# Kernel tuning notes

Measured on AMD Instinct MI355X. Metric: run time of the kernel, lower is better.

The kernel has to match this reference:

```python
import jax, jax.numpy as jnp
import numpy as np

N_AGENTS = 64
_adj = np.ones((N_AGENTS, N_AGENTS)) - np.eye(N_AGENTS)
SEND_NP, RECV_NP = np.where(_adj)  # 4032 directed edges, no self-loops
N_EDGES = SEND_NP.shape[0]

D_NODE = 16
H = 64
D_OUT = 16
N_TYPES = 2
BATCH = 128


def _glorot(key, shape):
    fan_in, fan_out = shape[0], shape[1]
    lim = np.sqrt(6.0 / (fan_in + fan_out)).astype(np.float32)
    return jax.random.uniform(key, shape, jnp.float32, -lim, lim)


def setup_inputs() -> dict:
    key = jax.random.key(0)
    ks = jax.random.split(key, 16)
    inp = {
        "node_states": jax.random.normal(ks[0], (BATCH, N_AGENTS, 1, D_NODE), jnp.float32),
        "edge_types": jax.random.uniform(ks[1], (BATCH, N_EDGES, N_TYPES + 1, 1), jnp.float32),
        # edge encoder 0: MLP(32 -> 64 -> 64)
        "e0_w1": _glorot(ks[2], (2 * D_NODE, H)), "e0_b1": jnp.zeros((H,), jnp.float32),
        "e0_w2": _glorot(ks[3], (H, H)), "e0_b2": jnp.zeros((H,), jnp.float32),
        # edge encoder 1
        "e1_w1": _glorot(ks[4], (2 * D_NODE, H)), "e1_b1": jnp.zeros((H,), jnp.float32),
        "e1_w2": _glorot(ks[5], (H, H)), "e1_b2": jnp.zeros((H,), jnp.float32),
        # node decoder: MLP(16+64 -> 64 -> 16)
        "nd_w1": _glorot(ks[6], (D_NODE + H, H)), "nd_b1": jnp.zeros((H,), jnp.float32),
        "nd_w2": _glorot(ks[7], (H, D_OUT)), "nd_b2": jnp.zeros((D_OUT,), jnp.float32),
    }
    return inp


def _mlp2(x, w1, b1, w2, b2):
    h = jax.nn.relu(x @ w1 + b1)
    return jax.nn.relu(h @ w2 + b2)


def reference(node_states, edge_types,
              e0_w1, e0_b1, e0_w2, e0_b2,
              e1_w1, e1_b1, e1_w2, e1_b2,
              nd_w1, nd_b1, nd_w2, nd_b2):
    send = jnp.asarray(SEND_NP)
    recv = jnp.asarray(RECV_NP)
    # NodeAggregator: gather sender/receiver states to edges -> [B, E, 1, 2D]
    edge_msg = jnp.concatenate([node_states[:, send], node_states[:, recv]], axis=-1)
    # per-edge-type MLP encode, concat along axis 2 -> [B, E, T, H]
    enc0 = _mlp2(edge_msg, e0_w1, e0_b1, e0_w2, e0_b2)
    enc1 = _mlp2(edge_msg, e1_w1, e1_b1, e1_w2, e1_b2)
    encoded = jnp.concatenate([enc0, enc1], axis=2)
    # masked sum over edge types (skip type-0 'no edge') -> [B, E, 1, H]
    edge_msg_sum = jnp.sum(encoded * edge_types[:, :, 1:, :], axis=2, keepdims=True)
    # EdgeAggregator: scatter-sum edge messages to receiver nodes -> [B, N, 1, H]
    node_msg = jax.ops.segment_sum(
        edge_msg_sum.swapaxes(0, 1), recv, num_segments=N_AGENTS).swapaxes(0, 1)
    # decode
    node_state = jnp.concatenate([node_states, node_msg], axis=-1)  # [B, N, 1, D+H]
    return _mlp2(node_state, nd_w1, nd_b1, nd_w2, nd_b2)
```

## Files before the change

### kernel.cpp

```cpp
#include <hip/hip_runtime.h>
#include <hip/hip_fp16.h>


typedef _Float16 hf;
typedef __attribute__((ext_vector_type(8))) _Float16 v8hf;
typedef __attribute__((ext_vector_type(4))) float fv4;

union ABh { v8hf v; __half2 h[4]; };

__global__ __launch_bounds__(256, 4) void fused_kernel(
    const float* __restrict__ ns, const float* __restrict__ et,
    const float* __restrict__ e0w1, const float* __restrict__ e0b1,
    const float* __restrict__ e0w2, const float* __restrict__ e0b2,
    const float* __restrict__ e1w1, const float* __restrict__ e1b1,
    const float* __restrict__ e1w2, const float* __restrict__ e1b2,
    const float* __restrict__ ndw1, const float* __restrict__ ndb1,
    const float* __restrict__ ndw2, const float* __restrict__ ndb2,
    float* __restrict__ out)
{
  __shared__ __align__(16) _Float16 PlH[2*64*72];
  __shared__ __align__(16) _Float16 QbH[2*8*64];
  __shared__ float ETl[2*8*64];
  __shared__ __align__(16) _Float16 XDH[24*104];
  _Float16* XD  = XDH;
  _Float16* HD2 = XDH + 8*104;

  int t = threadIdx.x;
  int b = blockIdx.x >> 3, rg = blockIdx.x & 7, r0 = rg*8;
  int w = t >> 6, lane = t & 63, quad = lane >> 4, col = lane & 15;

  const __half2 z2 = __float22half2_rn(make_float2(0.f, 0.f));
  const v8hf zero8 = {};

  float xnv = 0.f;
  if (t < 128) xnv = ns[(b*64 + r0 + (t >> 4))*16 + (t & 15)];
  float ev0[2], ev1[2];
  int es[2], erl[2];
#pragma unroll
  for (int i = 0; i < 2; ++i) {
    int idx = i*256 + t;
    int s = idx >> 3, rl = idx & 7;
    es[i] = s; erl[i] = rl;
    int r = r0 + rl;
    float v0 = 0.f, v1 = 0.f;
    if (s != r) {
      int pos = r - (r > s ? 1 : 0);
      const float* base = et + (b*4032 + s*63 + pos)*3;
      v0 = base[1]; v1 = base[2];
    }
    ev0[i] = v0; ev1[i] = v1;
  }

  {
    ABh a;
    if (quad < 2) {
      const float* xr = ns + (b*64 + w*16 + col)*16 + quad*8;
      float4 x0 = *(const float4*)xr;
      float4 x1 = *(const float4*)(xr + 4);
      a.h[0] = __float22half2_rn(make_float2(x0.x, x0.y));
      a.h[1] = __float22half2_rn(make_float2(x0.z, x0.w));
      a.h[2] = __float22half2_rn(make_float2(x1.x, x1.y));
      a.h[3] = __float22half2_rn(make_float2(x1.z, x1.w));
    } else {
      a.h[0] = a.h[1] = a.h[2] = a.h[3] = z2;
    }
    bool qwave = (w == (rg >> 1));
#pragma unroll 1
    for (int enc = 0; enc < 2; ++enc) {
      const float* w1 = enc ? e1w1 : e0w1;
      const float* b1 = enc ? e1b1 : e0b1;
#pragma unroll
      for (int ht = 0; ht < 4; ++ht) {
        int cc = ht*16 + col;
        ABh bb;
        if (quad < 2) {
#pragma unroll
          for (int j = 0; j < 4; ++j) {
            float f0 = w1[(quad*8 + 2*j    )*64 + cc];
            float f1 = w1[(quad*8 + 2*j + 1)*64 + cc];
            bb.h[j] = __float22half2_rn(make_float2(f0, f1));
          }
        } else {
          bb.h[0] = bb.h[1] = bb.h[2] = bb.h[3] = z2;
        }
        fv4 acc = {0.f, 0.f, 0.f, 0.f};
        acc = __builtin_amdgcn_mfma_f32_16x16x32_f16(a.v, bb.v, acc, 0, 0, 0);
        hf* pd = PlH + enc*4608 + (w*16 + quad*4)*72 + cc;
        pd[0*72] = (hf)acc[0];
        pd[1*72] = (hf)acc[1];
        pd[2*72] = (hf)acc[2];
        pd[3*72] = (hf)acc[3];
      }
      if (qwave) {
#pragma unroll
        for (int ht = 0; ht < 4; ++ht) {
          int cc = ht*16 + col;
          ABh bb;
          if (quad < 2) {
#pragma unroll
            for (int j = 0; j < 4; ++j) {
              float f0 = w1[(16 + quad*8 + 2*j    )*64 + cc];
              float f1 = w1[(16 + quad*8 + 2*j + 1)*64 + cc];
              bb.h[j] = __float22half2_rn(make_float2(f0, f1));
            }
          } else {
            bb.h[0] = bb.h[1] = bb.h[2] = bb.h[3] = z2;
          }
          fv4 acc = {0.f, 0.f, 0.f, 0.f};
          acc = __builtin_amdgcn_mfma_f32_16x16x32_f16(a.v, bb.v, acc, 0, 0, 0);
          float b1v = b1[cc];
#pragma unroll
          for (int rr = 0; rr < 4; ++rr) {
            int local = quad*4 + rr;
            if ((local >> 3) == (rg & 1))
              QbH[enc*512 + (local & 7)*64 + cc] = (hf)(acc[rr] + b1v);
          }
        }
      }
    }
  }
  if (t < 128) {
    int rl = t >> 4, k = t & 15;
    XD[rl*104 + k] = (hf)xnv;
    XD[rl*104 + 80 + k] = (hf)0.f;
  }
#pragma unroll
  for (int i = 0; i < 2; ++i) {
    ETl[erl[i]*64 + es[i]] = ev0[i];
    ETl[512 + erl[i]*64 + es[i]] = ev1[i];
  }
  __syncthreads();

  float msgacc[2][4] = {{0.f,0.f,0.f,0.f},{0.f,0.f,0.f,0.f}};

#pragma unroll 1
  for (int enc = 0; enc < 2; ++enc) {
    const float* w2 = enc ? e1w2 : e0w2;
    const float* b2 = enc ? e1b2 : e0b2;
    v8hf bfr[4][2];
    float b2v[4];
#pragma unroll
    for (int nt = 0; nt < 4; ++nt) {
#pragma unroll
      for (int kk = 0; kk < 2; ++kk) {
        const float* base = w2 + (kk*32 + quad*8)*64 + nt*16 + col;
        ABh bb;
        bb.h[0] = __float22half2_rn(make_float2(base[0*64], base[1*64]));
        bb.h[1] = __float22half2_rn(make_float2(base[2*64], base[3*64]));
        bb.h[2] = __float22half2_rn(make_float2(base[4*64], base[5*64]));
        bb.h[3] = __float22half2_rn(make_float2(base[6*64], base[7*64]));
        bfr[nt][kk] = bb.v;
      }
      b2v[nt] = b2[nt*16 + col];
    }
#pragma unroll 1
    for (int rli = 0; rli < 2; ++rli) {
      int rl = w*2 + rli;
      const hf* qrow = QbH + (enc*8 + rl)*64;
      v8hf q0 = *(const v8hf*)(qrow + quad*8);
      v8hf q1 = *(const v8hf*)(qrow + 32 + quad*8);
      const float* etrow = ETl + (enc*8 + rl)*64;
#pragma unroll 2
      for (int st = 0; st < 4; ++st) {
        const hf* prow = PlH + enc*4608 + (st*16 + col)*72 + quad*8;
        v8hf p0 = *(const v8hf*)prow;
        v8hf p1 = *(const v8hf*)(prow + 32);
        v8hf s0 = __builtin_elementwise_max(p0 + q0, zero8);
        v8hf s1 = __builtin_elementwise_max(p1 + q1, zero8);
        float4 etv = *(const float4*)(etrow + st*16 + quad*4);
#pragma unroll
        for (int nt = 0; nt < 4; ++nt) {
          fv4 acc = {b2v[nt], b2v[nt], b2v[nt], b2v[nt]};
          acc = __builtin_amdgcn_mfma_f32_16x16x32_f16(s0, bfr[nt][0], acc, 0, 0, 0);
          acc = __builtin_amdgcn_mfma_f32_16x16x32_f16(s1, bfr[nt][1], acc, 0, 0, 0);
          float m = msgacc[rli][nt];
          m += etv.x * fmaxf(acc[0], 0.f);
          m += etv.y * fmaxf(acc[1], 0.f);
          m += etv.z * fmaxf(acc[2], 0.f);
          m += etv.w * fmaxf(acc[3], 0.f);
          msgacc[rli][nt] = m;
        }
      }
    }
  }
#pragma unroll
  for (int rli = 0; rli < 2; ++rli) {
#pragma unroll
    for (int nt = 0; nt < 4; ++nt) {
      float v = msgacc[rli][nt];
      v += __shfl_xor(v, 16);
      v += __shfl_xor(v, 32);
      if (lane < 16) XD[(w*2 + rli)*104 + 16 + nt*16 + lane] = (hf)v;
    }
  }
  __syncthreads();

  if (w == 0) {
    ABh xa[3];
    const hf* xrow = XD + col*104;
#pragma unroll
    for (int kk = 0; kk < 3; ++kk) xa[kk].v = *(const v8hf*)(xrow + kk*32 + quad*8);
#pragma unroll
    for (int ht = 0; ht < 4; ++ht) {
      int cc = ht*16 + col;
      float bias = ndb1[cc];
      fv4 acc = {bias, bias, bias, bias};
#pragma unroll
      for (int kk = 0; kk < 3; ++kk) {
        ABh bb;
#pragma unroll
        for (int j = 0; j < 4; ++j) {
          int rA = kk*32 + quad*8 + 2*j;
          int rB = rA + 1;
          float f0 = ndw1[(rA < 80 ? rA : 79)*64 + cc] * (rA < 80 ? 1.f : 0.f);
          float f1 = ndw1[(rB < 80 ? rB : 79)*64 + cc] * (rB < 80 ? 1.f : 0.f);
          bb.h[j] = __float22half2_rn(make_float2(f0, f1));
        }
        acc = __builtin_amdgcn_mfma_f32_16x16x32_f16(xa[kk].v, bb.v, acc, 0, 0, 0);
      }
      if (quad < 2) {
#pragma unroll
        for (int rr = 0; rr < 4; ++rr)
          HD2[(quad*4 + rr)*104 + cc] = (hf)fmaxf(acc[rr], 0.f);
      }
    }
    const hf* hrow = HD2 + col*104;
    v8hf ha0 = *(const v8hf*)(hrow + quad*8);
    v8hf ha1 = *(const v8hf*)(hrow + 32 + quad*8);
    ABh b20, b21;
#pragma unroll
    for (int j = 0; j < 4; ++j) {
      float f0 = ndw2[(quad*8 + 2*j    )*16 + col];
      float f1 = ndw2[(quad*8 + 2*j + 1)*16 + col];
      b20.h[j] = __float22half2_rn(make_float2(f0, f1));
      float g0 = ndw2[(32 + quad*8 + 2*j    )*16 + col];
      float g1 = ndw2[(32 + quad*8 + 2*j + 1)*16 + col];
      b21.h[j] = __float22half2_rn(make_float2(g0, g1));
    }
    float bias2 = ndb2[col];
    fv4 acc2 = {bias2, bias2, bias2, bias2};
    acc2 = __builtin_amdgcn_mfma_f32_16x16x32_f16(ha0, b20.v, acc2, 0, 0, 0);
    acc2 = __builtin_amdgcn_mfma_f32_16x16x32_f16(ha1, b21.v, acc2, 0, 0, 0);
    if (quad < 2) {
#pragma unroll
      for (int rr = 0; rr < 4; ++rr) {
        int rl = quad*4 + rr;
        out[(b*64 + r0 + rl)*16 + col] = fmaxf(acc2[rr], 0.f);
      }
    }
  }
}

extern "C" void kernel_launch(void* const* d_in, const int* in_sizes, int n_in,
                              void* d_out, int out_size, void* d_ws, size_t ws_size,
                              hipStream_t stream) {
  const float* ns   = (const float*)d_in[0];
  const float* et   = (const float*)d_in[1];
  const float* e0w1 = (const float*)d_in[2];
  const float* e0b1 = (const float*)d_in[3];
  const float* e0w2 = (const float*)d_in[4];
  const float* e0b2 = (const float*)d_in[5];
  const float* e1w1 = (const float*)d_in[6];
  const float* e1b1 = (const float*)d_in[7];
  const float* e1w2 = (const float*)d_in[8];
  const float* e1b2 = (const float*)d_in[9];
  const float* ndw1 = (const float*)d_in[10];
  const float* ndb1 = (const float*)d_in[11];
  const float* ndw2 = (const float*)d_in[12];
  const float* ndb2 = (const float*)d_in[13];

  fused_kernel<<<1024, 256, 0, stream>>>(ns, et,
                                         e0w1, e0b1, e0w2, e0b2,
                                         e1w1, e1b1, e1w2, e1b2,
                                         ndw1, ndb1, ndw2, ndb2,
                                         (float*)d_out);
}
```

Baseline: 109.1 us.

## Stage weight matrices into LDS as transposed fp16 via coalesced float4 loads

Replaces the per-lane strided scalar global loads and fp16 conversions of all MLP weight matrices with a cooperative staging step. The block loads each matrix with coalesced float4 reads, converts it once to fp16 in a transposed, padded LDS layout, and the MFMA B operands are then read as single 16-byte LDS vectors. This targets uncoalesced global traffic and redundant conversions in every wave. In exchange it adds extra LDS (a new WB buffer), reuses PlH for the decoder weights, and inserts several more __syncthreads barriers, which may lower occupancy.

```diff
diff --git a/kernel.cpp b/kernel.cpp
--- a/kernel.cpp
+++ b/kernel.cpp
@@ -22,6 +22,7 @@
   __shared__ __align__(16) _Float16 QbH[2*8*64];
   __shared__ float ETl[2*8*64];
   __shared__ __align__(16) _Float16 XDH[24*104];
+  __shared__ __align__(16) _Float16 WB[2*64*40 + 16];
   _Float16* XD  = XDH;
   _Float16* HD2 = XDH + 8*104;
 
@@ -35,12 +36,10 @@
   float xnv = 0.f;
   if (t < 128) xnv = ns[(b*64 + r0 + (t >> 4))*16 + (t & 15)];
   float ev0[2], ev1[2];
-  int es[2], erl[2];
 #pragma unroll
   for (int i = 0; i < 2; ++i) {
     int idx = i*256 + t;
     int s = idx >> 3, rl = idx & 7;
-    es[i] = s; erl[i] = rl;
     int r = r0 + rl;
     float v0 = 0.f, v1 = 0.f;
     if (s != r) {
@@ -50,6 +49,24 @@
     }
     ev0[i] = v0; ev1[i] = v1;
   }
+
+#pragma unroll
+  for (int it = 0; it < 4; ++it) {
+    int idx = it*256 + t;
+    int enc = idx >> 9, rem = idx & 511;
+    int k = rem >> 4, h0 = (rem & 15)*4;
+    const float* w1 = enc ? e1w1 : e0w1;
+    float4 v = *(const float4*)(w1 + k*64 + h0);
+    hf* dst = WB + enc*2560 + h0*40 + k;
+    dst[0*40] = (hf)v.x; dst[1*40] = (hf)v.y; dst[2*40] = (hf)v.z; dst[3*40] = (hf)v.w;
+  }
+#pragma unroll
+  for (int d = 0; d < 4; ++d) {
+    int z = t*4 + d;
+    WB[(z >> 3)*40 + 32 + (z & 7)] = (hf)0.f;
+  }
+  if (t < 16) WB[5120 + t] = (hf)0.f;
+  __syncthreads();
 
   {
     ABh a;
@@ -67,24 +84,13 @@
     bool qwave = (w == (rg >> 1));
 #pragma unroll 1
     for (int enc = 0; enc < 2; ++enc) {
-      const float* w1 = enc ? e1w1 : e0w1;
       const float* b1 = enc ? e1b1 : e0b1;
 #pragma unroll
       for (int ht = 0; ht < 4; ++ht) {
         int cc = ht*16 + col;
-        ABh bb;
-        if (quad < 2) {
-#pragma unroll
-          for (int j = 0; j < 4; ++j) {
-            float f0 = w1[(quad*8 + 2*j    )*64 + cc];
-            float f1 = w1[(quad*8 + 2*j + 1)*64 + cc];
-            bb.h[j] = __float22half2_rn(make_float2(f0, f1));
-          }
-        } else {
-          bb.h[0] = bb.h[1] = bb.h[2] = bb.h[3] = z2;
-        }
+        v8hf bb = *(const v8hf*)(WB + enc*2560 + cc*40 + quad*8);
         fv4 acc = {0.f, 0.f, 0.f, 0.f};
-        acc = __builtin_amdgcn_mfma_f32_16x16x32_f16(a.v, bb.v, acc, 0, 0, 0);
+        acc = __builtin_amdgcn_mfma_f32_16x16x32_f16(a.v, bb, acc, 0, 0, 0);
         hf* pd = PlH + enc*4608 + (w*16 + quad*4)*72 + cc;
         pd[0*72] = (hf)acc[0];
         pd[1*72] = (hf)acc[1];
@@ -95,19 +101,9 @@
 #pragma unroll
         for (int ht = 0; ht < 4; ++ht) {
           int cc = ht*16 + col;
-          ABh bb;
-          if (quad < 2) {
-#pragma unroll
-            for (int j = 0; j < 4; ++j) {
-              float f0 = w1[(16 + quad*8 + 2*j    )*64 + cc];
-              float f1 = w1[(16 + quad*8 + 2*j + 1)*64 + cc];
-              bb.h[j] = __float22half2_rn(make_float2(f0, f1));
-            }
-          } else {
-            bb.h[0] = bb.h[1] = bb.h[2] = bb.h[3] = z2;
-          }
+          v8hf bb = *(const v8hf*)(WB + enc*2560 + cc*40 + 16 + quad*8);
           fv4 acc = {0.f, 0.f, 0.f, 0.f};
-          acc = __builtin_amdgcn_mfma_f32_16x16x32_f16(a.v, bb.v, acc, 0, 0, 0);
+          acc = __builtin_amdgcn_mfma_f32_16x16x32_f16(a.v, bb, acc, 0, 0, 0);
           float b1v = b1[cc];
 #pragma unroll
           for (int rr = 0; rr < 4; ++rr) {
@@ -119,6 +115,16 @@
       }
     }
   }
+  __syncthreads();
+
+#pragma unroll
+  for (int it = 0; it < 4; ++it) {
+    int idx = it*256 + t;
+    int k = idx >> 4, n0 = (idx & 15)*4;
+    float4 v = *(const float4*)(e0w2 + k*64 + n0);
+    hf* dst = WB + n0*72 + k;
+    dst[0*72] = (hf)v.x; dst[1*72] = (hf)v.y; dst[2*72] = (hf)v.z; dst[3*72] = (hf)v.w;
+  }
   if (t < 128) {
     int rl = t >> 4, k = t & 15;
     XD[rl*104 + k] = (hf)xnv;
@@ -126,8 +132,10 @@
   }
 #pragma unroll
   for (int i = 0; i < 2; ++i) {
-    ETl[erl[i]*64 + es[i]] = ev0[i];
-    ETl[512 + erl[i]*64 + es[i]] = ev1[i];
+    int idx = i*256 + t;
+    int s = idx >> 3, rl = idx & 7;
+    ETl[rl*64 + s] = ev0[i];
+    ETl[512 + rl*64 + s] = ev1[i];
   }
   __syncthreads();
 
@@ -135,22 +143,26 @@
 
 #pragma unroll 1
   for (int enc = 0; enc < 2; ++enc) {
-    const float* w2 = enc ? e1w2 : e0w2;
+    if (enc == 1) {
+      __syncthreads();
+#pragma unroll
+      for (int it = 0; it < 4; ++it) {
+        int idx = it*256 + t;
+        int k = idx >> 4, n0 = (idx & 15)*4;
+        float4 v = *(const float4*)(e1w2 + k*64 + n0);
+        hf* dst = WB + n0*72 + k;
+        dst[0*72] = (hf)v.x; dst[1*72] = (hf)v.y; dst[2*72] = (hf)v.z; dst[3*72] = (hf)v.w;
+      }
+      __syncthreads();
+    }
     const float* b2 = enc ? e1b2 : e0b2;
     v8hf bfr[4][2];
     float b2v[4];
 #pragma unroll
     for (int nt = 0; nt < 4; ++nt) {
 #pragma unroll
-      for (int kk = 0; kk < 2; ++kk) {
-        const float* base = w2 + (kk*32 + quad*8)*64 + nt*16 + col;
-        ABh bb;
-        bb.h[0] = __float22half2_rn(make_float2(base[0*64], base[1*64]));
-        bb.h[1] = __float22half2_rn(make_float2(base[2*64], base[3*64]));
-        bb.h[2] = __float22half2_rn(make_float2(base[4*64], base[5*64]));
-        bb.h[3] = __float22half2_rn(make_float2(base[6*64], base[7*64]));
-        bfr[nt][kk] = bb.v;
-      }
+      for (int kk = 0; kk < 2; ++kk)
+        bfr[nt][kk] = *(const v8hf*)(WB + (nt*16 + col)*72 + kk*32 + quad*8);
       b2v[nt] = b2[nt*16 + col];
     }
 #pragma unroll 1
@@ -195,6 +207,28 @@
   }
   __syncthreads();
 
+#pragma unroll
+  for (int it = 0; it < 5; ++it) {
+    int idx = it*256 + t;
+    int k = idx >> 4, n0 = (idx & 15)*4;
+    float4 v = *(const float4*)(ndw1 + k*64 + n0);
+    hf* dst = PlH + n0*104 + k;
+    dst[0*104] = (hf)v.x; dst[1*104] = (hf)v.y; dst[2*104] = (hf)v.z; dst[3*104] = (hf)v.w;
+  }
+#pragma unroll
+  for (int d = 0; d < 4; ++d) {
+    int z = t*4 + d;
+    PlH[(z >> 4)*104 + 80 + (z & 15)] = (hf)0.f;
+  }
+  {
+    int k = t >> 2, o0 = (t & 3)*4;
+    float4 v = *(const float4*)(ndw2 + k*16 + o0);
+    hf* nd2 = PlH + 6656;
+    nd2[(o0+0)*72 + k] = (hf)v.x; nd2[(o0+1)*72 + k] = (hf)v.y;
+    nd2[(o0+2)*72 + k] = (hf)v.z; nd2[(o0+3)*72 + k] = (hf)v.w;
+  }
+  __syncthreads();
+
   if (w == 0) {
     ABh xa[3];
     const hf* xrow = XD + col*104;
@@ -207,16 +241,8 @@
       fv4 acc = {bias, bias, bias, bias};
 #pragma unroll
       for (int kk = 0; kk < 3; ++kk) {
-        ABh bb;
-#pragma unroll
-        for (int j = 0; j < 4; ++j) {
-          int rA = kk*32 + quad*8 + 2*j;
-          int rB = rA + 1;
-          float f0 = ndw1[(rA < 80 ? rA : 79)*64 + cc] * (rA < 80 ? 1.f : 0.f);
-          float f1 = ndw1[(rB < 80 ? rB : 79)*64 + cc] * (rB < 80 ? 1.f : 0.f);
-          bb.h[j] = __float22half2_rn(make_float2(f0, f1));
-        }
-        acc = __builtin_amdgcn_mfma_f32_16x16x32_f16(xa[kk].v, bb.v, acc, 0, 0, 0);
+        v8hf bb = *(const v8hf*)(PlH + cc*104 + kk*32 + quad*8);
+        acc = __builtin_amdgcn_mfma_f32_16x16x32_f16(xa[kk].v, bb, acc, 0, 0, 0);
       }
       if (quad < 2) {
 #pragma unroll
@@ -227,20 +253,13 @@
     const hf* hrow = HD2 + col*104;
     v8hf ha0 = *(const v8hf*)(hrow + quad*8);
     v8hf ha1 = *(const v8hf*)(hrow + 32 + quad*8);
-    ABh b20, b21;
-#pragma unroll
-    for (int j = 0; j < 4; ++j) {
-      float f0 = ndw2[(quad*8 + 2*j    )*16 + col];
-      float f1 = ndw2[(quad*8 + 2*j + 1)*16 + col];
-      b20.h[j] = __float22half2_rn(make_float2(f0, f1));
-      float g0 = ndw2[(32 + quad*8 + 2*j    )*16 + col];
-      float g1 = ndw2[(32 + quad*8 + 2*j + 1)*16 + col];
-      b21.h[j] = __float22half2_rn(make_float2(g0, g1));
-    }
+    const hf* nd2 = PlH + 6656;
+    v8hf b20 = *(const v8hf*)(nd2 + col*72 + quad*8);
+    v8hf b21 = *(const v8hf*)(nd2 + col*72 + 32 + quad*8);
     float bias2 = ndb2[col];
     fv4 acc2 = {bias2, bias2, bias2, bias2};
-    acc2 = __builtin_amdgcn_mfma_f32_16x16x32_f16(ha0, b20.v, acc2, 0, 0, 0);
-    acc2 = __builtin_amdgcn_mfma_f32_16x16x32_f16(ha1, b21.v, acc2, 0, 0, 0);
+    acc2 = __builtin_amdgcn_mfma_f32_16x16x32_f16(ha0, b20, acc2, 0, 0, 0);
+    acc2 = __builtin_amdgcn_mfma_f32_16x16x32_f16(ha1, b21, acc2, 0, 0, 0);
     if (quad < 2) {
 #pragma unroll
       for (int rr = 0; rr < 4; ++rr) {
```

Result: slower. 112.3 us (+2.9%).

## Split fused kernel into sender-half message kernel plus separate decode kernel

Applied to the files above, without the earlier changes.

The message stage now splits each (batch, receiver-group) block into two blocks that each cover half of the senders. This doubles the grid and halves the shared-memory footprint, and occupancy is raised to 6 waves per SIMD. The per-sender first-layer projections are spread across the odd waves, and the even waves compute the receiver-bias term for one encoder each, which removes redundant and imbalanced work. Partial node messages go to a global workspace, and a second small kernel sums the two halves and runs the node decoder MLP. The cost is an extra launch and a global round trip of about 4 MB for the partial messages.

```diff
diff --git a/kernel.cpp b/kernel.cpp
--- a/kernel.cpp
+++ b/kernel.cpp
@@ -8,53 +8,47 @@
 
 union ABh { v8hf v; __half2 h[4]; };
 
-__global__ __launch_bounds__(256, 4) void fused_kernel(
+__global__ __launch_bounds__(256, 6) void k1_msg(
     const float* __restrict__ ns, const float* __restrict__ et,
     const float* __restrict__ e0w1, const float* __restrict__ e0b1,
     const float* __restrict__ e0w2, const float* __restrict__ e0b2,
     const float* __restrict__ e1w1, const float* __restrict__ e1b1,
     const float* __restrict__ e1w2, const float* __restrict__ e1b2,
-    const float* __restrict__ ndw1, const float* __restrict__ ndb1,
-    const float* __restrict__ ndw2, const float* __restrict__ ndb2,
-    float* __restrict__ out)
+    float* __restrict__ wsmsg)
 {
-  __shared__ __align__(16) _Float16 PlH[2*64*72];
+  __shared__ __align__(16) _Float16 PlH[2*32*72];
   __shared__ __align__(16) _Float16 QbH[2*8*64];
-  __shared__ float ETl[2*8*64];
-  __shared__ __align__(16) _Float16 XDH[24*104];
-  _Float16* XD  = XDH;
-  _Float16* HD2 = XDH + 8*104;
+  __shared__ float ETl[2*8*32];
 
   int t = threadIdx.x;
-  int b = blockIdx.x >> 3, rg = blockIdx.x & 7, r0 = rg*8;
+  int bid = blockIdx.x;
+  int b = bid >> 4, rg = (bid >> 1) & 7, sh = bid & 1;
+  int r0 = rg*8, s0 = sh*32;
   int w = t >> 6, lane = t & 63, quad = lane >> 4, col = lane & 15;
 
   const __half2 z2 = __float22half2_rn(make_float2(0.f, 0.f));
   const v8hf zero8 = {};
 
-  float xnv = 0.f;
-  if (t < 128) xnv = ns[(b*64 + r0 + (t >> 4))*16 + (t & 15)];
-  float ev0[2], ev1[2];
-  int es[2], erl[2];
-#pragma unroll
-  for (int i = 0; i < 2; ++i) {
-    int idx = i*256 + t;
-    int s = idx >> 3, rl = idx & 7;
-    es[i] = s; erl[i] = rl;
-    int r = r0 + rl;
+  {
+    int sl = t >> 3, rl = t & 7;
+    int s = s0 + sl, r = r0 + rl;
     float v0 = 0.f, v1 = 0.f;
     if (s != r) {
       int pos = r - (r > s ? 1 : 0);
       const float* base = et + (b*4032 + s*63 + pos)*3;
       v0 = base[1]; v1 = base[2];
     }
-    ev0[i] = v0; ev1[i] = v1;
+    ETl[rl*32 + sl] = v0;
+    ETl[256 + rl*32 + sl] = v1;
   }
 
   {
+    int nsrow = (w == 1) ? (s0 + col)
+              : (w == 3) ? (s0 + 16 + col)
+              : min(r0 + col, 63);
     ABh a;
     if (quad < 2) {
-      const float* xr = ns + (b*64 + w*16 + col)*16 + quad*8;
+      const float* xr = ns + (b*64 + nsrow)*16 + quad*8;
       float4 x0 = *(const float4*)xr;
       float4 x1 = *(const float4*)(xr + 4);
       a.h[0] = __float22half2_rn(make_float2(x0.x, x0.y));
@@ -64,34 +58,11 @@
     } else {
       a.h[0] = a.h[1] = a.h[2] = a.h[3] = z2;
     }
-    bool qwave = (w == (rg >> 1));
+    if (w & 1) {
+      int st = (w == 3);
 #pragma unroll 1
-    for (int enc = 0; enc < 2; ++enc) {
-      const float* w1 = enc ? e1w1 : e0w1;
-      const float* b1 = enc ? e1b1 : e0b1;
-#pragma unroll
-      for (int ht = 0; ht < 4; ++ht) {
-        int cc = ht*16 + col;
-        ABh bb;
-        if (quad < 2) {
-#pragma unroll
-          for (int j = 0; j < 4; ++j) {
-            float f0 = w1[(quad*8 + 2*j    )*64 + cc];
-            float f1 = w1[(quad*8 + 2*j + 1)*64 + cc];
-            bb.h[j] = __float22half2_rn(make_float2(f0, f1));
-          }
-        } else {
-          bb.h[0] = bb.h[1] = bb.h[2] = bb.h[3] = z2;
-        }
-        fv4 acc = {0.f, 0.f, 0.f, 0.f};
-        acc = __builtin_amdgcn_mfma_f32_16x16x32_f16(a.v, bb.v, acc, 0, 0, 0);
-        hf* pd = PlH + enc*4608 + (w*16 + quad*4)*72 + cc;
-        pd[0*72] = (hf)acc[0];
-        pd[1*72] = (hf)acc[1];
-        pd[2*72] = (hf)acc[2];
-        pd[3*72] = (hf)acc[3];
-      }
-      if (qwave) {
+      for (int enc = 0; enc < 2; ++enc) {
+        const float* w1 = enc ? e1w1 : e0w1;
 #pragma unroll
         for (int ht = 0; ht < 4; ++ht) {
           int cc = ht*16 + col;
@@ -99,8 +70,8 @@
           if (quad < 2) {
 #pragma unroll
             for (int j = 0; j < 4; ++j) {
-              float f0 = w1[(16 + quad*8 + 2*j    )*64 + cc];
-              float f1 = w1[(16 + quad*8 + 2*j + 1)*64 + cc];
+              float f0 = w1[(quad*8 + 2*j    )*64 + cc];
+              float f1 = w1[(quad*8 + 2*j + 1)*64 + cc];
               bb.h[j] = __float22half2_rn(make_float2(f0, f1));
             }
           } else {
@@ -108,26 +79,41 @@
           }
           fv4 acc = {0.f, 0.f, 0.f, 0.f};
           acc = __builtin_amdgcn_mfma_f32_16x16x32_f16(a.v, bb.v, acc, 0, 0, 0);
-          float b1v = b1[cc];
-#pragma unroll
-          for (int rr = 0; rr < 4; ++rr) {
-            int local = quad*4 + rr;
-            if ((local >> 3) == (rg & 1))
-              QbH[enc*512 + (local & 7)*64 + cc] = (hf)(acc[rr] + b1v);
+          hf* pd = PlH + enc*2304 + (st*16 + quad*4)*72 + cc;
+          pd[0*72] = (hf)acc[0];
+          pd[1*72] = (hf)acc[1];
+          pd[2*72] = (hf)acc[2];
+          pd[3*72] = (hf)acc[3];
+        }
+      }
+    } else {
+      int enc = (w == 2);
+      const float* w1 = enc ? e1w1 : e0w1;
+      const float* b1 = enc ? e1b1 : e0b1;
+#pragma unroll
+      for (int ht = 0; ht < 4; ++ht) {
+        int cc = ht*16 + col;
+        ABh bb;
+        if (quad < 2) {
+#pragma unroll
+          for (int j = 0; j < 4; ++j) {
+            float f0 = w1[(16 + quad*8 + 2*j    )*64 + cc];
+            float f1 = w1[(16 + quad*8 + 2*j + 1)*64 + cc];
+            bb.h[j] = __float22half2_rn(make_float2(f0, f1));
           }
-        }
-      }
-    }
-  }
-  if (t < 128) {
-    int rl = t >> 4, k = t & 15;
-    XD[rl*104 + k] = (hf)xnv;
-    XD[rl*104 + 80 + k] = (hf)0.f;
-  }
-#pragma unroll
-  for (int i = 0; i < 2; ++i) {
-    ETl[erl[i]*64 + es[i]] = ev0[i];
-    ETl[512 + erl[i]*64 + es[i]] = ev1[i];
+        } else {
+          bb.h[0] = bb.h[1] = bb.h[2] = bb.h[3] = z2;
+        }
+        fv4 acc = {0.f, 0.f, 0.f, 0.f};
+        acc = __builtin_amdgcn_mfma_f32_16x16x32_f16(a.v, bb.v, acc, 0, 0, 0);
+        float b1v = b1[cc];
+        if (quad < 2) {
+#pragma unroll
+          for (int rr = 0; rr < 4; ++rr)
+            QbH[enc*512 + (quad*4 + rr)*64 + cc] = (hf)(acc[rr] + b1v);
+        }
+      }
+    }
   }
   __syncthreads();
 
@@ -156,23 +142,23 @@
 #pragma unroll 1
     for (int rli = 0; rli < 2; ++rli) {
       int rl = w*2 + rli;
-      const hf* qrow = QbH + (enc*8 + rl)*64;
+      const hf* qrow = QbH + enc*512 + rl*64;
       v8hf q0 = *(const v8hf*)(qrow + quad*8);
       v8hf q1 = *(const v8hf*)(qrow + 32 + quad*8);
-      const float* etrow = ETl + (enc*8 + rl)*64;
-#pragma unroll 2
-      for (int st = 0; st < 4; ++st) {
-        const hf* prow = PlH + enc*4608 + (st*16 + col)*72 + quad*8;
+      const float* etrow = ETl + enc*256 + rl*32;
+#pragma unroll
+      for (int st = 0; st < 2; ++st) {
+        const hf* prow = PlH + enc*2304 + (st*16 + col)*72 + quad*8;
         v8hf p0 = *(const v8hf*)prow;
         v8hf p1 = *(const v8hf*)(prow + 32);
-        v8hf s0 = __builtin_elementwise_max(p0 + q0, zero8);
-        v8hf s1 = __builtin_elementwise_max(p1 + q1, zero8);
+        v8hf sA = __builtin_elementwise_max(p0 + q0, zero8);
+        v8hf sB = __builtin_elementwise_max(p1 + q1, zero8);
         float4 etv = *(const float4*)(etrow + st*16 + quad*4);
 #pragma unroll
         for (int nt = 0; nt < 4; ++nt) {
           fv4 acc = {b2v[nt], b2v[nt], b2v[nt], b2v[nt]};
-          acc = __builtin_amdgcn_mfma_f32_16x16x32_f16(s0, bfr[nt][0], acc, 0, 0, 0);
-          acc = __builtin_amdgcn_mfma_f32_16x16x32_f16(s1, bfr[nt][1], acc, 0, 0, 0);
+          acc = __builtin_amdgcn_mfma_f32_16x16x32_f16(sA, bfr[nt][0], acc, 0, 0, 0);
+          acc = __builtin_amdgcn_mfma_f32_16x16x32_f16(sB, bfr[nt][1], acc, 0, 0, 0);
           float m = msgacc[rli][nt];
           m += etv.x * fmaxf(acc[0], 0.f);
           m += etv.y * fmaxf(acc[1], 0.f);
@@ -190,64 +176,97 @@
       float v = msgacc[rli][nt];
       v += __shfl_xor(v, 16);
       v += __shfl_xor(v, 32);
-      if (lane < 16) XD[(w*2 + rli)*104 + 16 + nt*16 + lane] = (hf)v;
-    }
+      if (lane < 16) {
+        int r = rg*8 + w*2 + rli;
+        wsmsg[((sh*128 + b)*64 + r)*64 + nt*16 + lane] = v;
+      }
+    }
+  }
+}
+
+__global__ __launch_bounds__(64) void k2_decode(
+    const float* __restrict__ ns, const float* __restrict__ wsmsg,
+    const float* __restrict__ ndw1, const float* __restrict__ ndb1,
+    const float* __restrict__ ndw2, const float* __restrict__ ndb2,
+    float* __restrict__ out)
+{
+  __shared__ __align__(16) _Float16 HD[16*72];
+
+  int t = threadIdx.x;
+  int b = blockIdx.x >> 2, n0 = (blockIdx.x & 3)*16;
+  int quad = t >> 4, col = t & 15;
+
+  ABh xa[3];
+#pragma unroll
+  for (int kk = 0; kk < 3; ++kk) {
+    int k0 = kk*32 + quad*8;
+    ABh a;
+    if (k0 < 16) {
+      const float* p = ns + (b*64 + n0 + col)*16 + k0;
+      float4 u0 = *(const float4*)p, u1 = *(const float4*)(p + 4);
+      a.h[0] = __float22half2_rn(make_float2(u0.x, u0.y));
+      a.h[1] = __float22half2_rn(make_float2(u0.z, u0.w));
+      a.h[2] = __float22half2_rn(make_float2(u1.x, u1.y));
+      a.h[3] = __float22half2_rn(make_float2(u1.z, u1.w));
+    } else if (k0 < 80) {
+      int h = k0 - 16;
+      const float* p0 = wsmsg + ((0*128 + b)*64 + n0 + col)*64 + h;
+      const float* p1 = wsmsg + ((1*128 + b)*64 + n0 + col)*64 + h;
+      float4 u0 = *(const float4*)p0, u1 = *(const float4*)(p0 + 4);
+      float4 v0 = *(const float4*)p1, v1 = *(const float4*)(p1 + 4);
+      a.h[0] = __float22half2_rn(make_float2(u0.x + v0.x, u0.y + v0.y));
+      a.h[1] = __float22half2_rn(make_float2(u0.z + v0.z, u0.w + v0.w));
+      a.h[2] = __float22half2_rn(make_float2(u1.x + v1.x, u1.y + v1.y));
+      a.h[3] = __float22half2_rn(make_float2(u1.z + v1.z, u1.w + v1.w));
+    } else {
+      a.h[0] = a.h[1] = a.h[2] = a.h[3] = __float22half2_rn(make_float2(0.f, 0.f));
+    }
+    xa[kk] = a;
+  }
+#pragma unroll
+  for (int ht = 0; ht < 4; ++ht) {
+    int cc = ht*16 + col;
+    float bias = ndb1[cc];
+    fv4 acc = {bias, bias, bias, bias};
+#pragma unroll
+    for (int kk = 0; kk < 3; ++kk) {
+      ABh bb;
+#pragma unroll
+      for (int j = 0; j < 4; ++j) {
+        int rA = kk*32 + quad*8 + 2*j, rB = rA + 1;
+        float f0 = (rA < 80) ? ndw1[rA*64 + cc] : 0.f;
+        float f1 = (rB < 80) ? ndw1[rB*64 + cc] : 0.f;
+        bb.h[j] = __float22half2_rn(make_float2(f0, f1));
+      }
+      acc = __builtin_amdgcn_mfma_f32_16x16x32_f16(xa[kk].v, bb.v, acc, 0, 0, 0);
+    }
+#pragma unroll
+    for (int rr = 0; rr < 4; ++rr)
+      HD[(quad*4 + rr)*72 + cc] = (hf)fmaxf(acc[rr], 0.f);
   }
   __syncthreads();
 
-  if (w == 0) {
-    ABh xa[3];
-    const hf* xrow = XD + col*104;
-#pragma unroll
-    for (int kk = 0; kk < 3; ++kk) xa[kk].v = *(const v8hf*)(xrow + kk*32 + quad*8);
-#pragma unroll
-    for (int ht = 0; ht < 4; ++ht) {
-      int cc = ht*16 + col;
-      float bias = ndb1[cc];
-      fv4 acc = {bias, bias, bias, bias};
-#pragma unroll
-      for (int kk = 0; kk < 3; ++kk) {
-        ABh bb;
-#pragma unroll
-        for (int j = 0; j < 4; ++j) {
-          int rA = kk*32 + quad*8 + 2*j;
-          int rB = rA + 1;
-          float f0 = ndw1[(rA < 80 ? rA : 79)*64 + cc] * (rA < 80 ? 1.f : 0.f);
-          float f1 = ndw1[(rB < 80 ? rB : 79)*64 + cc] * (rB < 80 ? 1.f : 0.f);
-          bb.h[j] = __float22half2_rn(make_float2(f0, f1));
-        }
-        acc = __builtin_amdgcn_mfma_f32_16x16x32_f16(xa[kk].v, bb.v, acc, 0, 0, 0);
-      }
-      if (quad < 2) {
-#pragma unroll
-        for (int rr = 0; rr < 4; ++rr)
-          HD2[(quad*4 + rr)*104 + cc] = (hf)fmaxf(acc[rr], 0.f);
-      }
-    }
-    const hf* hrow = HD2 + col*104;
-    v8hf ha0 = *(const v8hf*)(hrow + quad*8);
-    v8hf ha1 = *(const v8hf*)(hrow + 32 + quad*8);
-    ABh b20, b21;
-#pragma unroll
-    for (int j = 0; j < 4; ++j) {
-      float f0 = ndw2[(quad*8 + 2*j    )*16 + col];
-      float f1 = ndw2[(quad*8 + 2*j + 1)*16 + col];
-      b20.h[j] = __float22half2_rn(make_float2(f0, f1));
-      float g0 = ndw2[(32 + quad*8 + 2*j    )*16 + col];
-      float g1 = ndw2[(32 + quad*8 + 2*j + 1)*16 + col];
-      b21.h[j] = __float22half2_rn(make_float2(g0, g1));
-    }
-    float bias2 = ndb2[col];
-    fv4 acc2 = {bias2, bias2, bias2, bias2};
-    acc2 = __builtin_amdgcn_mfma_f32_16x16x32_f16(ha0, b20.v, acc2, 0, 0, 0);
-    acc2 = __builtin_amdgcn_mfma_f32_16x16x32_f16(ha1, b21.v, acc2, 0, 0, 0);
-    if (quad < 2) {
-#pragma unroll
-      for (int rr = 0; rr < 4; ++rr) {
-        int rl = quad*4 + rr;
-        out[(b*64 + r0 + rl)*16 + col] = fmaxf(acc2[rr], 0.f);
-      }
-    }
+  const hf* hrow = HD + col*72;
+  v8hf ha0 = *(const v8hf*)(hrow + quad*8);
+  v8hf ha1 = *(const v8hf*)(hrow + 32 + quad*8);
+  ABh b20, b21;
+#pragma unroll
+  for (int j = 0; j < 4; ++j) {
+    float f0 = ndw2[(quad*8 + 2*j    )*16 + col];
+    float f1 = ndw2[(quad*8 + 2*j + 1)*16 + col];
+    b20.h[j] = __float22half2_rn(make_float2(f0, f1));
+    float g0 = ndw2[(32 + quad*8 + 2*j    )*16 + col];
+    float g1 = ndw2[(32 + quad*8 + 2*j + 1)*16 + col];
+    b21.h[j] = __float22half2_rn(make_float2(g0, g1));
+  }
+  float bias2 = ndb2[col];
+  fv4 acc2 = {bias2, bias2, bias2, bias2};
+  acc2 = __builtin_amdgcn_mfma_f32_16x16x32_f16(ha0, b20.v, acc2, 0, 0, 0);
+  acc2 = __builtin_amdgcn_mfma_f32_16x16x32_f16(ha1, b21.v, acc2, 0, 0, 0);
+#pragma unroll
+  for (int rr = 0; rr < 4; ++rr) {
+    int m = quad*4 + rr;
+    out[(b*64 + n0 + m)*16 + col] = fmaxf(acc2[rr], 0.f);
   }
 }
 
@@ -269,9 +288,12 @@
   const float* ndw2 = (const float*)d_in[12];
   const float* ndb2 = (const float*)d_in[13];
 
-  fused_kernel<<<1024, 256, 0, stream>>>(ns, et,
-                                         e0w1, e0b1, e0w2, e0b2,
-                                         e1w1, e1b1, e1w2, e1b2,
-                                         ndw1, ndb1, ndw2, ndb2,
-                                         (float*)d_out);
+  float* wsmsg = (float*)d_ws;
+
+  k1_msg<<<2048, 256, 0, stream>>>(ns, et,
+                                   e0w1, e0b1, e0w2, e0b2,
+                                   e1w1, e1b1, e1w2, e1b2,
+                                   wsmsg);
+  k2_decode<<<512, 64, 0, stream>>>(ns, wsmsg, ndw1, ndb1, ndw2, ndb2,
+                                    (float*)d_out);
 }
```

After: 261.6 us. +139.8%, slower.
